# Kernel optimization log

Hardware: AMD Instinct MI355X
Metric: run time of the kernel (lower is better)

The kernel has to match this reference:

```python
import jax, jax.numpy as jnp
import numpy as np

DIM = 1024
NUM_HEADS = 16
HEAD_DIM = DIM // NUM_HEADS
SCALE = HEAD_DIM ** -0.5
SIGMA_DATA = 1.0


def setup_inputs() -> dict:
    key = jax.random.key(0)
    ks = jax.random.split(key, 5)
    B, N = 2, 2048
    x = jax.random.normal(ks[0], (B, N, DIM), dtype=jnp.float32)
    t = jnp.asarray(0.5, dtype=jnp.float32)
    w_qkv = jax.random.normal(ks[1], (DIM, 3 * DIM), dtype=jnp.float32) * (DIM ** -0.5)
    b_qkv = jax.random.normal(ks[2], (3 * DIM,), dtype=jnp.float32) * 0.02
    w_proj = jax.random.normal(ks[3], (DIM, DIM), dtype=jnp.float32) * (DIM ** -0.5)
    b_proj = jax.random.normal(ks[4], (DIM,), dtype=jnp.float32) * 0.02
    return {"x": x, "t": t, "w_qkv": w_qkv, "b_qkv": b_qkv,
            "w_proj": w_proj, "b_proj": b_proj}


def reference(x, t, w_qkv, b_qkv, w_proj, b_proj):
    B, N, C = x.shape
    H, D = NUM_HEADS, HEAD_DIM
    # QKV projection: (B, N, 3C) -> (3, B, H, N, D)
    qkv = (x @ w_qkv + b_qkv).reshape(B, N, 3, H, D).transpose(2, 0, 3, 1, 4)
    q, k, v = qkv[0], qkv[1], qkv[2]
    # rCM skip coefficients (scalar t)
    sd2 = SIGMA_DATA ** 2
    t2 = t * t
    c_skip = sd2 / (t2 + sd2)
    c_out = SIGMA_DATA * t / jnp.sqrt(sd2 + t2)
    # Full (non-causal) softmax attention; the Triton kernel's online softmax
    # computes exactly the standard softmax (the 1e-6 l_i seed is annihilated
    # by alpha = exp(-1e9) on the first tile).
    scores = jnp.einsum('bhnd,bhmd->bhnm', q, k) * SCALE
    p = jax.nn.softmax(scores, axis=-1)
    attn = jnp.einsum('bhnm,bhmd->bhnd', p, v)
    # Skip-connection epilogue on per-head-reshaped x
    x_heads = x.reshape(B, N, H, D).transpose(0, 2, 1, 3)  # (B, H, N, D)
    out = c_skip * x_heads + c_out * attn
    out = out.transpose(0, 2, 1, 3).reshape(B, N, C)
    return out @ w_proj + b_proj
```

## Files before the change

kernel.cpp:

```cpp
#include <hip/hip_runtime.h>
#include <hip/hip_bf16.h>

typedef __attribute__((ext_vector_type(8))) short short8;
typedef __attribute__((ext_vector_type(4))) short short4b;
typedef __attribute__((ext_vector_type(4))) float float4v;
typedef __attribute__((ext_vector_type(8))) unsigned short ushort8v;

#define DIM 1024
#define NHEADS 16
#define HDIM 64
#define BATCH 2
#define SEQ 2048
#define LOG2E 1.4426950408889634f

__device__ __forceinline__ unsigned short f2bf(float f) {
    unsigned int u = __float_as_uint(f);
    unsigned int r = (u + 0x7fffu + ((u >> 16) & 1u)) >> 16;
    return (unsigned short)r;
}

__device__ __forceinline__ unsigned int cvt_pk_bf16(float lo, float hi) {
    unsigned int r;
    asm("v_cvt_pk_bf16_f32 %0, %1, %2" : "=v"(r) : "v"(lo), "v"(hi));
    return r;
}

__device__ __forceinline__ void gload_lds16(const void* g, void* l) {
    __builtin_amdgcn_global_load_lds(
        (const __attribute__((address_space(1))) void*)g,
        (__attribute__((address_space(3))) void*)l,
        16, 0, 0);
}

typedef __attribute__((address_space(3))) const unsigned short* lds_us_cp;

template<int OFF>
__device__ __forceinline__ short4b ds_tr16(const unsigned short* p) {
    short4b r;
    asm volatile("ds_read_b64_tr_b16 %0, %1 offset:%2"
                 : "=v"(r) : "v"((lds_us_cp)p), "i"(OFF));
    return r;
}

__global__ __launch_bounds__(256) void cast_x_kernel(const float* __restrict__ x,
                                                     unsigned short* __restrict__ xb) {
    int i = (blockIdx.x * 256 + threadIdx.x) * 8;
    float4 a = *(const float4*)(x + i);
    float4 b = *(const float4*)(x + i + 4);
    ushort8v o;
    o[0] = f2bf(a.x); o[1] = f2bf(a.y); o[2] = f2bf(a.z); o[3] = f2bf(a.w);
    o[4] = f2bf(b.x); o[5] = f2bf(b.y); o[6] = f2bf(b.z); o[7] = f2bf(b.w);
    *(ushort8v*)(xb + i) = o;
}

__global__ __launch_bounds__(256) void tcast_kernel(const float* __restrict__ W,
                                                    unsigned short* __restrict__ Wt,
                                                    int K, int N) {
    __shared__ float tile[32][33];
    int tx = threadIdx.x & 31, ty = threadIdx.x >> 5;
    int n0 = blockIdx.x * 32, k0 = blockIdx.y * 32;
#pragma unroll
    for (int i = 0; i < 4; ++i)
        tile[ty + i * 8][tx] = W[(size_t)(k0 + ty + i * 8) * N + n0 + tx];
    __syncthreads();
#pragma unroll
    for (int i = 0; i < 4; ++i)
        Wt[(size_t)(n0 + ty + i * 8) * K + k0 + tx] = f2bf(tile[tx][ty + i * 8]);
}

__global__ __launch_bounds__(256) void gemm_qkv_kernel(
    const unsigned short* __restrict__ A, const unsigned short* __restrict__ Bt,
    const float* __restrict__ bias,
    unsigned short* __restrict__ qb, unsigned short* __restrict__ kb,
    unsigned short* __restrict__ vb) {
    __shared__ unsigned short As[128 * 32];
    __shared__ unsigned short Bs[128 * 32];
    __shared__ unsigned short Cs[128 * 136];
    const int t = threadIdx.x;
    const int lane = t & 63;
    const int w = t >> 6;
    const int wr = w >> 1, wc = w & 1;
    const int lg = lane >> 4, lr = lane & 15;
    const int m0 = blockIdx.y * 128;
    const int n0 = blockIdx.x * 128;
    const int K = 1024;

    float4v acc[4][4] = {};

    for (int k0 = 0; k0 < K; k0 += 32) {
#pragma unroll
        for (int i = 0; i < 2; ++i) {
            int slot = i * 256 + t;
            int row = slot >> 2;
            int cb = (slot & 3) * 16;
            gload_lds16((const char*)(A + (size_t)(m0 + row) * K + k0) + cb,
                        (char*)As + slot * 16);
            gload_lds16((const char*)(Bt + (size_t)(n0 + row) * K + k0) + cb,
                        (char*)Bs + slot * 16);
        }
        __syncthreads();
        short8 af[4], bf[4];
#pragma unroll
        for (int m = 0; m < 4; ++m)
            af[m] = *(const short8*)(As + (wr * 64 + m * 16 + lr) * 32 + lg * 8);
#pragma unroll
        for (int n = 0; n < 4; ++n)
            bf[n] = *(const short8*)(Bs + (wc * 64 + n * 16 + lr) * 32 + lg * 8);
#pragma unroll
        for (int m = 0; m < 4; ++m)
#pragma unroll
            for (int n = 0; n < 4; ++n)
                acc[m][n] = __builtin_amdgcn_mfma_f32_16x16x32_bf16(af[m], bf[n], acc[m][n], 0, 0, 0);
        __syncthreads();
    }

    const int which = n0 >> 10;
    unsigned short* dst = (which == 0) ? qb : ((which == 1) ? kb : vb);
    const float sc = (which == 0) ? 0.125f * LOG2E : 1.0f;

#pragma unroll
    for (int n = 0; n < 4; ++n) {
        int col = wc * 64 + n * 16 + lr;
        float bv = bias[n0 + col];
#pragma unroll
        for (int m = 0; m < 4; ++m) {
#pragma unroll
            for (int r = 0; r < 4; ++r) {
                int row = wr * 64 + m * 16 + lg * 4 + r;
                Cs[row * 136 + col] = f2bf((acc[m][n][r] + bv) * sc);
            }
        }
    }
    __syncthreads();

    const int colh0 = n0 & 1023;
#pragma unroll
    for (int it = 0; it < 8; ++it) {
        int seg = it * 32 + (t >> 3);
        int row = seg >> 1, hh = seg & 1, chunk = t & 7;
        int grow = m0 + row;
        int b = grow >> 11, nn = grow & 2047;
        int colh = colh0 + hh * 64;
        int h = colh >> 6;
        int d = chunk * 8;
        ushort8v vv = *(const ushort8v*)(Cs + row * 136 + hh * 64 + d);
        *(ushort8v*)(&dst[((size_t)(b * NHEADS + h) * SEQ + nn) * HDIM + d]) = vv;
    }
}

__global__ __launch_bounds__(256) void attn_kernel(
    const unsigned short* __restrict__ q, const unsigned short* __restrict__ k,
    const unsigned short* __restrict__ v, const float* __restrict__ x,
    const float* __restrict__ tptr, unsigned short* __restrict__ y) {
    __shared__ unsigned short Ks[2][64 * 64];
    __shared__ unsigned short Vt[2][64 * 64];
    const int t = threadIdx.x;
    const int lane = t & 63;
    const int w = t >> 6;
    const int lg = lane >> 4, lr = lane & 15;
    const int bh = blockIdx.y;
    const int b = bh >> 4, h = bh & 15;
    const int q0 = blockIdx.x * 64 + w * 16;
    const size_t head_off = (size_t)bh * SEQ * HDIM;
    const unsigned short* qh = q + head_off;
    const unsigned short* kh = k + head_off;
    const unsigned short* vh = v + head_off;
    const int NT = SEQ / 64;

    short8 qf[2];
#pragma unroll
    for (int ks = 0; ks < 2; ++ks)
        qf[ks] = *(const short8*)(qh + (size_t)(q0 + lr) * HDIM + ks * 32 + lg * 8);

    union { unsigned short u[8]; short8 s8; } ones;
#pragma unroll
    for (int j = 0; j < 8; ++j) ones.u[j] = 0x3F80;

    float4v acc[4] = {};
    float4v acc_l = {};

    auto stage = [&](int tile, int buf) {
        const char* ktile = (const char*)(kh + (size_t)tile * 64 * HDIM);
#pragma unroll
        for (int i = 0; i < 2; ++i) {
            int slot = (i * 256 + t) * 16;
            int row = slot >> 7;
            int src = slot ^ ((row & 7) << 4);
            gload_lds16(ktile + src, (char*)Ks[buf] + slot);
        }
        const unsigned short* vt0 = vh + (size_t)tile * 64 * HDIM;
#pragma unroll
        for (int i = 0; i < 2; ++i) {
            int s = i * 256 + t;
            int st = s >> 3, g = s & 7;
            int db = st >> 4, kvg = st & 15;
            int kv = kvg * 4 + (g >> 1);
            int d = db * 16 + (g & 1) * 8;
            gload_lds16((const char*)(vt0 + (size_t)kv * HDIM + d),
                        (char*)Vt[buf] + s * 16);
        }
    };

    stage(0, 0);
    __syncthreads();

    for (int tt = 0; tt < NT; ++tt) {
        const int cur = tt & 1, nxt = cur ^ 1;

        if (tt + 1 < NT) stage(tt + 1, nxt);

        float4v s[4];
        __builtin_amdgcn_s_setprio(1);
#pragma unroll
        for (int n = 0; n < 4; ++n) {
            s[n] = (float4v){0.f, 0.f, 0.f, 0.f};
#pragma unroll
            for (int ks = 0; ks < 2; ++ks) {
                int row = n * 16 + lr;
                int byte = (row * 128 + (ks * 32 + lg * 8) * 2) ^ ((row & 7) << 4);
                short8 kf = *(const short8*)((const char*)Ks[cur] + byte);
                s[n] = __builtin_amdgcn_mfma_f32_16x16x32_bf16(kf, qf[ks], s[n], 0, 0, 0);
            }
        }
        __builtin_amdgcn_s_setprio(0);

#pragma unroll
        for (int n = 0; n < 4; ++n)
#pragma unroll
            for (int r = 0; r < 4; ++r)
                s[n][r] = exp2f(s[n][r]);

        const unsigned short* vbase = Vt[cur] + (size_t)lane * 4;
#pragma unroll
        for (int ks = 0; ks < 2; ++ks) {
            union { unsigned int u[4]; short8 s8; } pu;
            pu.u[0] = cvt_pk_bf16(s[2 * ks][0], s[2 * ks][1]);
            pu.u[1] = cvt_pk_bf16(s[2 * ks][2], s[2 * ks][3]);
            pu.u[2] = cvt_pk_bf16(s[2 * ks + 1][0], s[2 * ks + 1][1]);
            pu.u[3] = cvt_pk_bf16(s[2 * ks + 1][2], s[2 * ks + 1][3]);

            short4b lo0, hi0, lo1, hi1, lo2, hi2, lo3, hi3;
            if (ks == 0) {
                lo0 = ds_tr16<0>(vbase);    hi0 = ds_tr16<512>(vbase);
                lo1 = ds_tr16<2048>(vbase); hi1 = ds_tr16<2560>(vbase);
                lo2 = ds_tr16<4096>(vbase); hi2 = ds_tr16<4608>(vbase);
                lo3 = ds_tr16<6144>(vbase); hi3 = ds_tr16<6656>(vbase);
            } else {
                lo0 = ds_tr16<1024>(vbase); hi0 = ds_tr16<1536>(vbase);
                lo1 = ds_tr16<3072>(vbase); hi1 = ds_tr16<3584>(vbase);
                lo2 = ds_tr16<5120>(vbase); hi2 = ds_tr16<5632>(vbase);
                lo3 = ds_tr16<7168>(vbase); hi3 = ds_tr16<7680>(vbase);
            }
            asm volatile("s_waitcnt lgkmcnt(0)" ::: "memory");
            __builtin_amdgcn_sched_barrier(0);

            __builtin_amdgcn_s_setprio(1);
            acc[0] = __builtin_amdgcn_mfma_f32_16x16x32_bf16(
                pu.s8, __builtin_shufflevector(lo0, hi0, 0, 1, 2, 3, 4, 5, 6, 7), acc[0], 0, 0, 0);
            acc[1] = __builtin_amdgcn_mfma_f32_16x16x32_bf16(
                pu.s8, __builtin_shufflevector(lo1, hi1, 0, 1, 2, 3, 4, 5, 6, 7), acc[1], 0, 0, 0);
            acc[2] = __builtin_amdgcn_mfma_f32_16x16x32_bf16(
                pu.s8, __builtin_shufflevector(lo2, hi2, 0, 1, 2, 3, 4, 5, 6, 7), acc[2], 0, 0, 0);
            acc[3] = __builtin_amdgcn_mfma_f32_16x16x32_bf16(
                pu.s8, __builtin_shufflevector(lo3, hi3, 0, 1, 2, 3, 4, 5, 6, 7), acc[3], 0, 0, 0);
            acc_l = __builtin_amdgcn_mfma_f32_16x16x32_bf16(
                pu.s8, ones.s8, acc_l, 0, 0, 0);
            __builtin_amdgcn_s_setprio(0);
        }

        __syncthreads();
    }

    float tv = *tptr;
    float c_skip = 1.0f / (tv * tv + 1.0f);
    float c_out = tv * rsqrtf(1.0f + tv * tv);
#pragma unroll
    for (int vn = 0; vn < 4; ++vn) {
#pragma unroll
        for (int r = 0; r < 4; ++r) {
            int n = blockIdx.x * 64 + w * 16 + lg * 4 + r;
            int c = h * 64 + vn * 16 + lr;
            size_t off = (size_t)(b * SEQ + n) * DIM + c;
            float av = acc[vn][r] / acc_l[r];
            float o = c_skip * x[off] + c_out * av;
            y[off] = f2bf(o);
        }
    }
}

__global__ __launch_bounds__(256) void gemm_proj_kernel(
    const unsigned short* __restrict__ A, const unsigned short* __restrict__ Bt,
    const float* __restrict__ bias, float* __restrict__ out) {
    __shared__ unsigned short As[64 * 32];
    __shared__ unsigned short Bs[64 * 32];
    const int t = threadIdx.x;
    const int lane = t & 63;
    const int w = t >> 6;
    const int wr = w >> 1, wc = w & 1;
    const int lg = lane >> 4, lr = lane & 15;
    const int m0 = blockIdx.y * 64;
    const int n0 = blockIdx.x * 64;
    const int K = 1024;

    float4v acc[2][2] = {};

    for (int k0 = 0; k0 < K; k0 += 32) {
        {
            int slot = t;
            int row = slot >> 2;
            int cb = (slot & 3) * 16;
            gload_lds16((const char*)(A + (size_t)(m0 + row) * K + k0) + cb,
                        (char*)As + slot * 16);
            gload_lds16((const char*)(Bt + (size_t)(n0 + row) * K + k0) + cb,
                        (char*)Bs + slot * 16);
        }
        __syncthreads();
        short8 af[2], bf[2];
#pragma unroll
        for (int m = 0; m < 2; ++m)
            af[m] = *(const short8*)(As + (wr * 32 + m * 16 + lr) * 32 + lg * 8);
#pragma unroll
        for (int n = 0; n < 2; ++n)
            bf[n] = *(const short8*)(Bs + (wc * 32 + n * 16 + lr) * 32 + lg * 8);
#pragma unroll
        for (int m = 0; m < 2; ++m)
#pragma unroll
            for (int n = 0; n < 2; ++n)
                acc[m][n] = __builtin_amdgcn_mfma_f32_16x16x32_bf16(af[m], bf[n], acc[m][n], 0, 0, 0);
        __syncthreads();
    }

#pragma unroll
    for (int n = 0; n < 2; ++n) {
        int col = n0 + wc * 32 + n * 16 + lr;
        float bv = bias[col];
#pragma unroll
        for (int m = 0; m < 2; ++m) {
#pragma unroll
            for (int r = 0; r < 4; ++r) {
                int row = m0 + wr * 32 + m * 16 + lg * 4 + r;
                out[(size_t)row * DIM + col] = acc[m][n][r] + bv;
            }
        }
    }
}

extern "C" void kernel_launch(void* const* d_in, const int* in_sizes, int n_in,
                              void* d_out, int out_size, void* d_ws, size_t ws_size,
                              hipStream_t stream) {
    const float* x      = (const float*)d_in[0];
    const float* tsc    = (const float*)d_in[1];
    const float* w_qkv  = (const float*)d_in[2];
    const float* b_qkv  = (const float*)d_in[3];
    const float* w_proj = (const float*)d_in[4];
    const float* b_proj = (const float*)d_in[5];
    float* out = (float*)d_out;

    char* ws = (char*)d_ws;
    unsigned short* xb     = (unsigned short*)(ws);
    unsigned short* wqkvT  = (unsigned short*)(ws + 8388608);
    unsigned short* wprojT = (unsigned short*)(ws + 14680064);
    unsigned short* qb     = (unsigned short*)(ws + 16777216);
    unsigned short* kb     = (unsigned short*)(ws + 25165824);
    unsigned short* vb     = (unsigned short*)(ws + 33554432);
    unsigned short* yb     = (unsigned short*)(ws + 41943040);

    cast_x_kernel<<<2048, 256, 0, stream>>>(x, xb);
    tcast_kernel<<<dim3(96, 32), 256, 0, stream>>>(w_qkv, wqkvT, 1024, 3072);
    tcast_kernel<<<dim3(32, 32), 256, 0, stream>>>(w_proj, wprojT, 1024, 1024);
    gemm_qkv_kernel<<<dim3(24, 32), 256, 0, stream>>>(xb, wqkvT, b_qkv, qb, kb, vb);
    attn_kernel<<<dim3(32, 32), 256, 0, stream>>>(qb, kb, vb, x, tsc, yb);
    gemm_proj_kernel<<<dim3(16, 64), 256, 0, stream>>>(yb, wprojT, b_proj, out);
}
```

Baseline: 208.3 us.

## Triple-buffer K/V tiles in attention with a single barrier per iteration

Moves the attention kernel's K/V staging from double buffering to three LDS buffers with rotating pointers, prefetching two tiles ahead. It waits on vmcnt for the oldest tile and uses one raw s_barrier per iteration instead of two __syncthreads. The aim is to hide global-to-LDS latency better and cut synchronization. The cost is 50% more LDS per block, which may lower occupancy, and correctness now rests on the hand-counted vmcnt values.

```diff
diff --git a/kernel.cpp b/kernel.cpp
--- a/kernel.cpp
+++ b/kernel.cpp
@@ -152,8 +152,8 @@
     const unsigned short* __restrict__ q, const unsigned short* __restrict__ k,
     const unsigned short* __restrict__ v, const float* __restrict__ x,
     const float* __restrict__ tptr, unsigned short* __restrict__ y) {
-    __shared__ unsigned short Ks[2][64 * 64];
-    __shared__ unsigned short Vt[2][64 * 64];
+    __shared__ unsigned short Ks[3][64 * 64];
+    __shared__ unsigned short Vt[3][64 * 64];
     const int t = threadIdx.x;
     const int lane = t & 63;
     const int w = t >> 6;
@@ -179,14 +179,14 @@
     float4v acc[4] = {};
     float4v acc_l = {};
 
-    auto stage = [&](int tile, int buf) {
+    auto stage = [&](int tile, unsigned short* kd, unsigned short* vd) {
         const char* ktile = (const char*)(kh + (size_t)tile * 64 * HDIM);
 #pragma unroll
         for (int i = 0; i < 2; ++i) {
             int slot = (i * 256 + t) * 16;
             int row = slot >> 7;
             int src = slot ^ ((row & 7) << 4);
-            gload_lds16(ktile + src, (char*)Ks[buf] + slot);
+            gload_lds16(ktile + src, (char*)kd + slot);
         }
         const unsigned short* vt0 = vh + (size_t)tile * 64 * HDIM;
 #pragma unroll
@@ -197,17 +197,22 @@
             int kv = kvg * 4 + (g >> 1);
             int d = db * 16 + (g & 1) * 8;
             gload_lds16((const char*)(vt0 + (size_t)kv * HDIM + d),
-                        (char*)Vt[buf] + s * 16);
+                        (char*)vd + s * 16);
         }
     };
 
-    stage(0, 0);
-    __syncthreads();
+    unsigned short *ksA = Ks[0], *ksB = Ks[1], *ksC = Ks[2];
+    unsigned short *vtA = Vt[0], *vtB = Vt[1], *vtC = Vt[2];
+
+    stage(0, ksA, vtA);
+    stage(1, ksB, vtB);
 
     for (int tt = 0; tt < NT; ++tt) {
-        const int cur = tt & 1, nxt = cur ^ 1;
-
-        if (tt + 1 < NT) stage(tt + 1, nxt);
+        if (tt == NT - 1) { asm volatile("s_waitcnt vmcnt(0)" ::: "memory"); }
+        else              { asm volatile("s_waitcnt vmcnt(4)" ::: "memory"); }
+        __builtin_amdgcn_s_barrier();
+
+        if (tt + 2 < NT) stage(tt + 2, ksC, vtC);
 
         float4v s[4];
         __builtin_amdgcn_s_setprio(1);
@@ -218,7 +223,7 @@
             for (int ks = 0; ks < 2; ++ks) {
                 int row = n * 16 + lr;
                 int byte = (row * 128 + (ks * 32 + lg * 8) * 2) ^ ((row & 7) << 4);
-                short8 kf = *(const short8*)((const char*)Ks[cur] + byte);
+                short8 kf = *(const short8*)((const char*)ksA + byte);
                 s[n] = __builtin_amdgcn_mfma_f32_16x16x32_bf16(kf, qf[ks], s[n], 0, 0, 0);
             }
         }
@@ -230,7 +235,7 @@
             for (int r = 0; r < 4; ++r)
                 s[n][r] = exp2f(s[n][r]);
 
-        const unsigned short* vbase = Vt[cur] + (size_t)lane * 4;
+        const unsigned short* vbase = vtA + (size_t)lane * 4;
 #pragma unroll
         for (int ks = 0; ks < 2; ++ks) {
             union { unsigned int u[4]; short8 s8; } pu;
@@ -268,12 +273,13 @@
             __builtin_amdgcn_s_setprio(0);
         }
 
-        __syncthreads();
-    }
-
-    float tv = *tptr;
-    float c_skip = 1.0f / (tv * tv + 1.0f);
-    float c_out = tv * rsqrtf(1.0f + tv * tv);
+        unsigned short* tk = ksA; ksA = ksB; ksB = ksC; ksC = tk;
+        unsigned short* tv = vtA; vtA = vtB; vtB = vtC; vtC = tv;
+    }
+
+    float tv2 = *tptr;
+    float c_skip = 1.0f / (tv2 * tv2 + 1.0f);
+    float c_out = tv2 * rsqrtf(1.0f + tv2 * tv2);
 #pragma unroll
     for (int vn = 0; vn < 4; ++vn) {
 #pragma unroll
```

Result: no change. 208.9 us (+0.3%).
